# Performance work log

Hardware: AMD Instinct MI355X
Metric: run time of the kernel (lower is better)

## Reference

```python
import jax, jax.numpy as jnp
import numpy as np

N_HEAD = 16


def setup_inputs() -> dict:
    key = jax.random.key(0)
    ks = jax.random.split(key, 6)
    B, T, H = 4, 2048, 1024
    inp = jax.random.normal(ks[0], (B, T, H), dtype=jnp.float32)
    # padding mask: valid prefix of random length in [T//2, T] per batch row
    lengths = jax.random.randint(ks[1], (B, 1), T // 2, T + 1)
    mask = jnp.arange(T)[None, :] < lengths  # (B, T) bool
    s = 0.02
    w_qkv = jax.random.normal(ks[2], (H, 3 * H), dtype=jnp.float32) * s
    b_qkv = jax.random.normal(ks[3], (3 * H,), dtype=jnp.float32) * s
    w_out = jax.random.normal(ks[4], (H, H), dtype=jnp.float32) * s
    b_out = jax.random.normal(ks[5], (H,), dtype=jnp.float32) * s
    return {"input": inp, "mask": mask, "w_qkv": w_qkv, "b_qkv": b_qkv,
            "w_out": w_out, "b_out": b_out}


def reference(input, mask, w_qkv, b_qkv, w_out, b_out):
    B, T, H = input.shape
    hd = H // N_HEAD
    qkv = input @ w_qkv + b_qkv                       # (B, T, 3H)
    q, k, v = jnp.split(qkv, 3, axis=-1)
    # (B, T, H) -> (B, nh, T, hd)
    q = q.reshape(B, T, N_HEAD, hd).transpose(0, 2, 1, 3)
    k = k.reshape(B, T, N_HEAD, hd).transpose(0, 2, 1, 3)
    v = v.reshape(B, T, N_HEAD, hd).transpose(0, 2, 1, 3)
    scores = jnp.einsum('bhqd,bhkd->bhqk', q, k) / jnp.sqrt(jnp.float32(hd))
    causal = jnp.tril(jnp.ones((T, T), dtype=bool))   # (T, T)
    full_mask = causal[None, None, :, :] & mask[:, None, None, :]  # (B,1,T,T) bcast over heads
    scores = jnp.where(full_mask, scores, -jnp.inf)
    attn = jax.nn.softmax(scores, axis=-1)            # (B, nh, T, T)
    o = jnp.einsum('bhqk,bhkd->bhqd', attn, v)        # (B, nh, T, hd)
    o = o.transpose(0, 2, 1, 3).reshape(B, T, H)
    return o @ w_out + b_out
```

## Files before the change

### kernel.cpp

```cpp
#include <hip/hip_runtime.h>
#include <math.h>

#define B_  4
#define T_  2048
#define H_  1024
#define NH  16
#define HD  64
#define H3  3072

typedef short bf16x8 __attribute__((ext_vector_type(8)));
typedef float f32x4  __attribute__((ext_vector_type(4)));

#define SC2F 0.18033688011112042f

__device__ __forceinline__ unsigned short f2bf(float f) {
    union { float f; unsigned u; } v; v.f = f;
    unsigned u = v.u;
    unsigned r = (u + 0x7fffu + ((u >> 16) & 1u)) >> 16;
    return (unsigned short)r;
}

__device__ __forceinline__ void gload_lds16(const void* g, void* l) {
    __builtin_amdgcn_global_load_lds(
        (const __attribute__((address_space(1))) unsigned*)g,
        (__attribute__((address_space(3))) unsigned*)l, 16, 0, 0);
}

__global__ void lengths_kernel(const void* mask, int* lengths) {
    int b = blockIdx.x;
    int t = threadIdx.x;
    const unsigned* mu = (const unsigned*)mask;
    bool is_byte = (mu[0] == 0x01010101u);
    int cnt = 0;
    if (is_byte) {
        const unsigned char* m8 = (const unsigned char*)mask;
        for (int i = t; i < T_; i += 256) cnt += (m8[b * T_ + i] != 0);
    } else {
        const unsigned* m32 = (const unsigned*)mask;
        for (int i = t; i < T_; i += 256) cnt += (m32[b * T_ + i] != 0);
    }
    __shared__ int red[256];
    red[t] = cnt;
    __syncthreads();
    for (int s = 128; s > 0; s >>= 1) {
        if (t < s) red[t] += red[t + s];
        __syncthreads();
    }
    if (t == 0) lengths[b] = red[0];
}

__global__ void convert_bf16_kernel(const float* __restrict__ x,
                                    unsigned short* __restrict__ y, int n) {
    int i = (blockIdx.x * 256 + threadIdx.x) * 4;
    if (i < n) {
        float4 v = *(const float4*)(x + i);
        ushort4 o;
        o.x = f2bf(v.x); o.y = f2bf(v.y); o.z = f2bf(v.z); o.w = f2bf(v.w);
        *(ushort4*)(y + i) = o;
    }
}

__global__ void transpose_bf16_kernel(const float* __restrict__ in,
                                      unsigned short* __restrict__ out,
                                      int K, int N) {
    __shared__ unsigned short tile[32][33];
    int kb = blockIdx.y * 32, nb = blockIdx.x * 32;
    int tx = threadIdx.x, ty = threadIdx.y;
    for (int i = 0; i < 32; i += 8)
        tile[ty + i][tx] = f2bf(in[(long)(kb + ty + i) * N + nb + tx]);
    __syncthreads();
    for (int i = 0; i < 32; i += 8)
        out[(long)(nb + ty + i) * K + kb + tx] = tile[tx][ty + i];
}

__global__ void vtranspose_kernel(const unsigned short* __restrict__ QKV,
                                  unsigned short* __restrict__ Vt) {
    int idx = blockIdx.x;
    int tt = idx & 31, bh = idx >> 5;
    int b = bh >> 4, h = bh & 15;
    __shared__ unsigned short Ls[64][72];
    int tid = threadIdx.x;
    {
        int row = tid >> 2, cb = (tid & 3) * 16;
        const unsigned short* src = QKV + ((long)(b * T_ + tt * 64 + row)) * H3 + 2 * H_ + h * HD + cb;
        *(float4*)(&Ls[row][cb])     = *(const float4*)(src);
        *(float4*)(&Ls[row][cb + 8]) = *(const float4*)(src + 8);
    }
    __syncthreads();
    {
        int d = tid >> 2, cb = (tid & 3) * 16;
        __align__(16) unsigned short tmp[16];
#pragma unroll
        for (int e = 0; e < 16; e++) tmp[e] = Ls[cb + e][d];
        unsigned short* dst = Vt + ((long)(bh * 64 + d)) * T_ + tt * 64 + cb;
        *(float4*)(dst)     = *(const float4*)(tmp);
        *(float4*)(dst + 8) = *(const float4*)(tmp + 8);
    }
}

template <bool BF16_OUT, bool KSCALE>
__global__ __launch_bounds__(256) void gemm_kernel(
    const unsigned short* __restrict__ A,
    const unsigned short* __restrict__ Bt,
    const float* __restrict__ bias,
    void* __restrict__ C,
    int M, int N, int K)
{
    __shared__ unsigned short Asm[128][64];
    __shared__ unsigned short Bsm[128][64];

    int tn = blockIdx.x * 128, tm = blockIdx.y * 128;
    int tid = threadIdx.x;
    int wid = tid >> 6, lane = tid & 63, quad = lane >> 4, lr = lane & 15;
    int wm = (wid & 1) * 64, wn = (wid >> 1) * 64;

    int rl = lane >> 3, cs = (lane & 7) ^ rl;
    const unsigned short* aP = A  + (long)(tm + wid * 32 + rl) * K + cs * 8;
    const unsigned short* bP = Bt + (long)(tn + wid * 32 + rl) * K + cs * 8;
    int xk = lr & 7;

    f32x4 acc[4][4] = {};

    for (int k0 = 0; k0 < K; k0 += 64) {
        __syncthreads();
#pragma unroll
        for (int t = 0; t < 4; t++) {
            gload_lds16(aP + (long)t * 8 * K + k0, &Asm[wid * 32 + t * 8][0]);
            gload_lds16(bP + (long)t * 8 * K + k0, &Bsm[wid * 32 + t * 8][0]);
        }
        __syncthreads();

#pragma unroll
        for (int hh = 0; hh < 2; hh++) {
            int pc = ((hh * 4 + quad) ^ xk) * 8;
            bf16x8 af[4], bfv[4];
#pragma unroll
            for (int i = 0; i < 4; i++) af[i]  = *(const bf16x8*)(&Asm[wm + i * 16 + lr][pc]);
#pragma unroll
            for (int j = 0; j < 4; j++) bfv[j] = *(const bf16x8*)(&Bsm[wn + j * 16 + lr][pc]);
#pragma unroll
            for (int i = 0; i < 4; i++)
#pragma unroll
                for (int j = 0; j < 4; j++)
                    acc[i][j] = __builtin_amdgcn_mfma_f32_16x16x32_bf16(af[i], bfv[j], acc[i][j], 0, 0, 0);
        }
    }

#pragma unroll
    for (int i = 0; i < 4; i++)
#pragma unroll
        for (int j = 0; j < 4; j++) {
            int col = tn + wn + j * 16 + lr;
            float bs = bias[col];
            bool ks = KSCALE && (col >= H_) && (col < 2 * H_);
#pragma unroll
            for (int r = 0; r < 4; r++) {
                int row = tm + wm + i * 16 + quad * 4 + r;
                float v = acc[i][j][r] + bs;
                if (ks) v *= SC2F;
                if (BF16_OUT)
                    ((unsigned short*)C)[(long)row * N + col] = f2bf(v);
                else
                    ((float*)C)[(long)row * N + col] = v;
            }
        }
}

__global__ __launch_bounds__(256) void attn_kernel(
    const unsigned short* __restrict__ QKV,
    const unsigned short* __restrict__ Vt,
    const int* __restrict__ lengths,
    unsigned short* __restrict__ O)
{
    int idx = blockIdx.x;
    int bh = idx & 63;
    int pr = idx >> 6;
    int b = bh >> 4, h = bh & 15;
    int len = lengths[b];

    int tid = threadIdx.x;
    int wid = tid >> 6, lane = tid & 63, quad = lane >> 4, lr = lane & 15;

    __shared__ unsigned short Qs[128][72];
    __shared__ unsigned short Ks[64][72];
    __shared__ unsigned short Vts[64][72];

    const long qkv_base = (long)b * T_ * H3;
    int srow = tid >> 2, scb = (tid & 3) * 16;

    for (int pass = 0; pass < 2; pass++) {
        int qt = pass ? pr : (15 - pr);
        int q0 = qt * 128;

        __syncthreads();
        {
            int row = tid >> 1, cb = (tid & 1) * 32;
            const unsigned short* src = QKV + qkv_base + (long)(q0 + row) * H3 + h * HD + cb;
#pragma unroll
            for (int i = 0; i < 4; i++)
                *(float4*)(&Qs[row][cb + i * 8]) = *(const float4*)(src + i * 8);
        }
        __syncthreads();

        bf16x8 qf[2][2];
#pragma unroll
        for (int nq = 0; nq < 2; nq++)
#pragma unroll
            for (int ks = 0; ks < 2; ks++)
                qf[nq][ks] = *(const bf16x8*)(&Qs[wid * 32 + nq * 16 + lr][ks * 32 + quad * 8]);

        float l_i[2] = { 0.f, 0.f };
        f32x4 Oacc[4][2] = {};

        int kmax = min(q0 + 127, len - 1);
        int n_kt = (kmax >> 6) + 1;
        int q_wave_lo = q0 + wid * 32;
        int q_wave_hi = q_wave_lo + 31;
        int myq[2] = { q_wave_lo + lr, q_wave_lo + 16 + lr };

        const unsigned short* kp = QKV + qkv_base + (long)srow * H3 + H_ + h * HD + scb;
        const unsigned short* vp = Vt + ((long)(bh * 64 + srow)) * T_ + scb;

        for (int kt = 0; kt < n_kt; kt++) {
            __syncthreads();
            *(float4*)(&Ks[srow][scb])      = *(const float4*)(kp);
            *(float4*)(&Ks[srow][scb + 8])  = *(const float4*)(kp + 8);
            *(float4*)(&Vts[srow][scb])     = *(const float4*)(vp);
            *(float4*)(&Vts[srow][scb + 8]) = *(const float4*)(vp + 8);
            kp += (long)64 * H3;
            vp += 64;
            __syncthreads();

            int k_lo = kt * 64;
            if (k_lo > q_wave_hi || k_lo >= len) continue;

            f32x4 Sacc[4][2] = {};
#pragma unroll
            for (int ks = 0; ks < 2; ks++) {
#pragma unroll
                for (int mt = 0; mt < 4; mt++) {
                    bf16x8 kf = *(const bf16x8*)(&Ks[mt * 16 + lr][ks * 32 + quad * 8]);
                    Sacc[mt][0] = __builtin_amdgcn_mfma_f32_16x16x32_bf16(kf, qf[0][ks], Sacc[mt][0], 0, 0, 0);
                    Sacc[mt][1] = __builtin_amdgcn_mfma_f32_16x16x32_bf16(kf, qf[1][ks], Sacc[mt][1], 0, 0, 0);
                }
            }

            bool full = (k_lo + 63 <= q_wave_lo) && (k_lo + 63 < len);
            float rs[2] = { 0.f, 0.f };
            unsigned pk[4][2][2];
#pragma unroll
            for (int mt = 0; mt < 4; mt++)
#pragma unroll
                for (int nq = 0; nq < 2; nq++) {
                    float p[4];
#pragma unroll
                    for (int r = 0; r < 4; r++) {
                        float s = Sacc[mt][nq][r];
                        if (!full) {
                            int key = k_lo + mt * 16 + quad * 4 + r;
                            bool ok = (key <= myq[nq]) && (key < len);
                            s = ok ? s : -INFINITY;
                        }
                        p[r] = __builtin_amdgcn_exp2f(s);
                        rs[nq] += p[r];
                    }
                    pk[mt][nq][0] = __builtin_amdgcn_perm(__float_as_uint(p[1]), __float_as_uint(p[0]), 0x07060302);
                    pk[mt][nq][1] = __builtin_amdgcn_perm(__float_as_uint(p[3]), __float_as_uint(p[2]), 0x07060302);
                }

#pragma unroll
            for (int nq = 0; nq < 2; nq++) {
                float v = rs[nq];
                v += __shfl_xor(v, 16);
                v += __shfl_xor(v, 32);
                l_i[nq] += v;
            }

            int src0 = ((quad & 1) * 2) * 16 + lr;
            int src1 = src0 + 16;
            bool hi = (quad >> 1) != 0;
#pragma unroll
            for (int ks = 0; ks < 2; ks++) {
                bf16x8 vf[4];
#pragma unroll
                for (int md = 0; md < 4; md++)
                    vf[md] = *(const bf16x8*)(&Vts[md * 16 + lr][ks * 32 + quad * 8]);
#pragma unroll
                for (int nq = 0; nq < 2; nq++) {
                    unsigned w0a = (unsigned)__shfl((int)pk[ks * 2][nq][0], src0);
                    unsigned w0b = (unsigned)__shfl((int)pk[ks * 2 + 1][nq][0], src0);
                    unsigned w1a = (unsigned)__shfl((int)pk[ks * 2][nq][1], src0);
                    unsigned w1b = (unsigned)__shfl((int)pk[ks * 2 + 1][nq][1], src0);
                    unsigned w2a = (unsigned)__shfl((int)pk[ks * 2][nq][0], src1);
                    unsigned w2b = (unsigned)__shfl((int)pk[ks * 2 + 1][nq][0], src1);
                    unsigned w3a = (unsigned)__shfl((int)pk[ks * 2][nq][1], src1);
                    unsigned w3b = (unsigned)__shfl((int)pk[ks * 2 + 1][nq][1], src1);
                    union { unsigned w[4]; bf16x8 v; } bu;
                    bu.w[0] = hi ? w0b : w0a;
                    bu.w[1] = hi ? w1b : w1a;
                    bu.w[2] = hi ? w2b : w2a;
                    bu.w[3] = hi ? w3b : w3a;
#pragma unroll
                    for (int md = 0; md < 4; md++)
                        Oacc[md][nq] = __builtin_amdgcn_mfma_f32_16x16x32_bf16(vf[md], bu.v, Oacc[md][nq], 0, 0, 0);
                }
            }
        }

        {
            float inv[2] = { 1.f / l_i[0], 1.f / l_i[1] };
#pragma unroll
            for (int nq = 0; nq < 2; nq++)
#pragma unroll
                for (int md = 0; md < 4; md++)
#pragma unroll
                    for (int rp = 0; rp < 2; rp++) {
                        float e0 = Oacc[md][nq][rp * 2]     * inv[nq];
                        float e1 = Oacc[md][nq][rp * 2 + 1] * inv[nq];
                        unsigned w = __builtin_amdgcn_perm(__float_as_uint(e1), __float_as_uint(e0), 0x07060302);
                        *(unsigned*)(&Qs[wid * 32 + nq * 16 + lr][md * 16 + quad * 4 + rp * 2]) = w;
                    }
            __asm__ volatile("s_waitcnt lgkmcnt(0)" ::: "memory");
            int row = lane >> 1, cb = (lane & 1) * 32;
            long tok = (long)b * T_ + q0 + wid * 32 + row;
#pragma unroll
            for (int i = 0; i < 4; i++) {
                float4 v = *(const float4*)(&Qs[wid * 32 + row][cb + i * 8]);
                *(float4*)(&O[tok * H_ + h * HD + cb + i * 8]) = v;
            }
        }
    }
}

extern "C" void kernel_launch(void* const* d_in, const int* in_sizes, int n_in,
                              void* d_out, int out_size, void* d_ws, size_t ws_size,
                              hipStream_t stream) {
    const float* X    = (const float*)d_in[0];
    const void*  mask = d_in[1];
    const float* Wqkv = (const float*)d_in[2];
    const float* bqkv = (const float*)d_in[3];
    const float* Wout = (const float*)d_in[4];
    const float* bout = (const float*)d_in[5];

    char* ws = (char*)d_ws;
    int* lengths          = (int*)ws;
    unsigned short* WqkvT = (unsigned short*)(ws + 256);
    unsigned short* WoutT = WqkvT + (long)H3 * H_;
    unsigned short* QKV   = WoutT + (long)H_ * H_;
    unsigned short* Xbf   = QKV + (long)B_ * T_ * H3;
    unsigned short* Vt    = Xbf + (long)B_ * T_ * H_;
    unsigned short* Obf   = Xbf;

    const int M = B_ * T_;

    lengths_kernel<<<B_, 256, 0, stream>>>(mask, lengths);
    convert_bf16_kernel<<<(M * H_ / 4 + 255) / 256, 256, 0, stream>>>(X, Xbf, M * H_);
    transpose_bf16_kernel<<<dim3(H3 / 32, H_ / 32), dim3(32, 8), 0, stream>>>(Wqkv, WqkvT, H_, H3);
    transpose_bf16_kernel<<<dim3(H_ / 32, H_ / 32), dim3(32, 8), 0, stream>>>(Wout, WoutT, H_, H_);
    gemm_kernel<true, true><<<dim3(H3 / 128, M / 128), 256, 0, stream>>>(Xbf, WqkvT, bqkv, QKV, M, H3, H_);
    vtranspose_kernel<<<B_ * NH * (T_ / 64), 256, 0, stream>>>(QKV, Vt);
    attn_kernel<<<B_ * NH * 8, 256, 0, stream>>>(QKV, Vt, lengths, Obf);
    gemm_kernel<false, false><<<dim3(H_ / 128, M / 128), 256, 0, stream>>>(Obf, WoutT, bout, d_out, M, H_, H_);
}
```

Baseline: 297.7 us.

## Fuse V transpose into QKV GEMM epilogue and double-buffer attention K/V tiles

The QKV GEMM now writes the V columns directly into a transposed Vt layout in its epilogue, which removes the separate vtranspose kernel and its extra pass over memory. The GEMM k-step is cut from 64 to 32 and drops the XOR swizzle on shared memory, which may add LDS bank conflicts and more barriers per unit of work. The attention kernel double-buffers K/V tiles with register prefetch so there is one barrier per tile instead of two. It also replaces the shuffle-based P repacking with 16x16x16 MFMAs that consume the softmax output layout directly.

```diff
diff --git a/kernel.cpp b/kernel.cpp
--- a/kernel.cpp
+++ b/kernel.cpp
@@ -9,6 +9,7 @@
 #define H3  3072
 
 typedef short bf16x8 __attribute__((ext_vector_type(8)));
+typedef short bf16x4 __attribute__((ext_vector_type(4)));
 typedef float f32x4  __attribute__((ext_vector_type(4)));
 
 #define SC2F 0.18033688011112042f
@@ -24,6 +25,19 @@
     __builtin_amdgcn_global_load_lds(
         (const __attribute__((address_space(1))) unsigned*)g,
         (__attribute__((address_space(3))) unsigned*)l, 16, 0, 0);
+}
+
+__device__ __forceinline__ f32x4 mfma_16x16x16_bf16(bf16x4 a, bf16x4 b, f32x4 c) {
+#if __has_builtin(__builtin_amdgcn_mfma_f32_16x16x16_bf16)
+    return __builtin_amdgcn_mfma_f32_16x16x16_bf16(a, b, c, 0, 0, 0);
+#elif __has_builtin(__builtin_amdgcn_mfma_f32_16x16x16bf16_1k)
+    return __builtin_amdgcn_mfma_f32_16x16x16bf16_1k(a, b, c, 0, 0, 0);
+#else
+    f32x4 d;
+    asm volatile("v_mfma_f32_16x16x16_bf16 %0, %1, %2, %3"
+                 : "=v"(d) : "v"(a), "v"(b), "v"(c));
+    return d;
+#endif
 }
 
 __global__ void lengths_kernel(const void* mask, int* lengths) {
@@ -73,77 +87,66 @@
         out[(long)(nb + ty + i) * K + kb + tx] = tile[tx][ty + i];
 }
 
-__global__ void vtranspose_kernel(const unsigned short* __restrict__ QKV,
-                                  unsigned short* __restrict__ Vt) {
-    int idx = blockIdx.x;
-    int tt = idx & 31, bh = idx >> 5;
-    int b = bh >> 4, h = bh & 15;
-    __shared__ unsigned short Ls[64][72];
-    int tid = threadIdx.x;
-    {
-        int row = tid >> 2, cb = (tid & 3) * 16;
-        const unsigned short* src = QKV + ((long)(b * T_ + tt * 64 + row)) * H3 + 2 * H_ + h * HD + cb;
-        *(float4*)(&Ls[row][cb])     = *(const float4*)(src);
-        *(float4*)(&Ls[row][cb + 8]) = *(const float4*)(src + 8);
-    }
-    __syncthreads();
-    {
-        int d = tid >> 2, cb = (tid & 3) * 16;
-        __align__(16) unsigned short tmp[16];
-#pragma unroll
-        for (int e = 0; e < 16; e++) tmp[e] = Ls[cb + e][d];
-        unsigned short* dst = Vt + ((long)(bh * 64 + d)) * T_ + tt * 64 + cb;
-        *(float4*)(dst)     = *(const float4*)(tmp);
-        *(float4*)(dst + 8) = *(const float4*)(tmp + 8);
-    }
-}
-
-template <bool BF16_OUT, bool KSCALE>
+template <bool BF16_OUT, bool KSCALE, bool VSPLIT>
 __global__ __launch_bounds__(256) void gemm_kernel(
     const unsigned short* __restrict__ A,
     const unsigned short* __restrict__ Bt,
     const float* __restrict__ bias,
     void* __restrict__ C,
+    unsigned short* __restrict__ Vt,
     int M, int N, int K)
 {
-    __shared__ unsigned short Asm[128][64];
-    __shared__ unsigned short Bsm[128][64];
+    __shared__ unsigned short Asm[128][32];
+    __shared__ unsigned short Bsm[128][32];
 
     int tn = blockIdx.x * 128, tm = blockIdx.y * 128;
     int tid = threadIdx.x;
     int wid = tid >> 6, lane = tid & 63, quad = lane >> 4, lr = lane & 15;
     int wm = (wid & 1) * 64, wn = (wid >> 1) * 64;
-
-    int rl = lane >> 3, cs = (lane & 7) ^ rl;
-    const unsigned short* aP = A  + (long)(tm + wid * 32 + rl) * K + cs * 8;
-    const unsigned short* bP = Bt + (long)(tn + wid * 32 + rl) * K + cs * 8;
-    int xk = lr & 7;
+    int grow = lane >> 2, gcol = (lane & 3) * 8;
 
     f32x4 acc[4][4] = {};
 
-    for (int k0 = 0; k0 < K; k0 += 64) {
-        __syncthreads();
-#pragma unroll
-        for (int t = 0; t < 4; t++) {
-            gload_lds16(aP + (long)t * 8 * K + k0, &Asm[wid * 32 + t * 8][0]);
-            gload_lds16(bP + (long)t * 8 * K + k0, &Bsm[wid * 32 + t * 8][0]);
-        }
-        __syncthreads();
-
-#pragma unroll
-        for (int hh = 0; hh < 2; hh++) {
-            int pc = ((hh * 4 + quad) ^ xk) * 8;
-            bf16x8 af[4], bfv[4];
-#pragma unroll
-            for (int i = 0; i < 4; i++) af[i]  = *(const bf16x8*)(&Asm[wm + i * 16 + lr][pc]);
-#pragma unroll
-            for (int j = 0; j < 4; j++) bfv[j] = *(const bf16x8*)(&Bsm[wn + j * 16 + lr][pc]);
-#pragma unroll
-            for (int i = 0; i < 4; i++)
-#pragma unroll
-                for (int j = 0; j < 4; j++)
-                    acc[i][j] = __builtin_amdgcn_mfma_f32_16x16x32_bf16(af[i], bfv[j], acc[i][j], 0, 0, 0);
-        }
+    for (int k0 = 0; k0 < K; k0 += 32) {
+        __syncthreads();
+#pragma unroll
+        for (int t = 0; t < 2; t++) {
+            int ar = wid * 32 + t * 16 + grow;
+            gload_lds16(A  + (long)(tm + ar) * K + k0 + gcol, &Asm[wid * 32 + t * 16][0]);
+            gload_lds16(Bt + (long)(tn + ar) * K + k0 + gcol, &Bsm[wid * 32 + t * 16][0]);
+        }
+        __syncthreads();
+
+        bf16x8 af[4], bfv[4];
+#pragma unroll
+        for (int i = 0; i < 4; i++) af[i]  = *(const bf16x8*)(&Asm[wm + i * 16 + lr][quad * 8]);
+#pragma unroll
+        for (int j = 0; j < 4; j++) bfv[j] = *(const bf16x8*)(&Bsm[wn + j * 16 + lr][quad * 8]);
+#pragma unroll
+        for (int i = 0; i < 4; i++)
+#pragma unroll
+            for (int j = 0; j < 4; j++)
+                acc[i][j] = __builtin_amdgcn_mfma_f32_16x16x32_bf16(af[i], bfv[j], acc[i][j], 0, 0, 0);
+    }
+
+    if (VSPLIT && tn >= 2 * H_) {
+#pragma unroll
+        for (int i = 0; i < 4; i++)
+#pragma unroll
+            for (int j = 0; j < 4; j++) {
+                int col = tn + wn + j * 16 + lr;
+                float bs = bias[col];
+                int feat = col - 2 * H_;
+                int tok0 = tm + wm + i * 16 + quad * 4;
+                int bb = tok0 >> 11;
+                unsigned d0 = (unsigned)f2bf(acc[i][j][0] + bs) |
+                              ((unsigned)f2bf(acc[i][j][1] + bs) << 16);
+                unsigned d1 = (unsigned)f2bf(acc[i][j][2] + bs) |
+                              ((unsigned)f2bf(acc[i][j][3] + bs) << 16);
+                unsigned short* dst = Vt + ((long)(bb * 1024 + feat)) * T_ + (tok0 & (T_ - 1));
+                *(uint2*)dst = make_uint2(d0, d1);
+            }
+        return;
     }
 
 #pragma unroll
@@ -182,11 +185,13 @@
     int wid = tid >> 6, lane = tid & 63, quad = lane >> 4, lr = lane & 15;
 
     __shared__ unsigned short Qs[128][72];
-    __shared__ unsigned short Ks[64][72];
-    __shared__ unsigned short Vts[64][72];
+    __shared__ unsigned short Kd[2][64][72];
+    __shared__ unsigned short Vd[2][64][72];
 
     const long qkv_base = (long)b * T_ * H3;
     int srow = tid >> 2, scb = (tid & 3) * 16;
+    const unsigned short* kbase = QKV + qkv_base + (long)srow * H3 + H_ + h * HD + scb;
+    const unsigned short* vbase = Vt + ((long)(bh * 64 + srow)) * T_ + scb;
 
     for (int pass = 0; pass < 2; pass++) {
         int qt = pass ? pr : (15 - pr);
@@ -199,6 +204,16 @@
 #pragma unroll
             for (int i = 0; i < 4; i++)
                 *(float4*)(&Qs[row][cb + i * 8]) = *(const float4*)(src + i * 8);
+        }
+        {
+            float4 k0 = *(const float4*)(kbase);
+            float4 k1 = *(const float4*)(kbase + 8);
+            float4 v0 = *(const float4*)(vbase);
+            float4 v1 = *(const float4*)(vbase + 8);
+            *(float4*)(&Kd[0][srow][scb])     = k0;
+            *(float4*)(&Kd[0][srow][scb + 8]) = k1;
+            *(float4*)(&Vd[0][srow][scb])     = v0;
+            *(float4*)(&Vd[0][srow][scb + 8]) = v1;
         }
         __syncthreads();
 
@@ -218,93 +233,87 @@
         int q_wave_hi = q_wave_lo + 31;
         int myq[2] = { q_wave_lo + lr, q_wave_lo + 16 + lr };
 
-        const unsigned short* kp = QKV + qkv_base + (long)srow * H3 + H_ + h * HD + scb;
-        const unsigned short* vp = Vt + ((long)(bh * 64 + srow)) * T_ + scb;
+        const unsigned short* kp = kbase + (long)64 * H3;
+        const unsigned short* vp = vbase + 64;
 
         for (int kt = 0; kt < n_kt; kt++) {
+            int cur = kt & 1;
+            float4 pk0, pk1, pv0, pv1;
+            bool pf = (kt + 1 < n_kt);
+            if (pf) {
+                pk0 = *(const float4*)(kp);
+                pk1 = *(const float4*)(kp + 8);
+                pv0 = *(const float4*)(vp);
+                pv1 = *(const float4*)(vp + 8);
+                kp += (long)64 * H3;
+                vp += 64;
+            }
+
+            int k_lo = kt * 64;
+            if (!(k_lo > q_wave_hi || k_lo >= len)) {
+                f32x4 Sacc[4][2] = {};
+#pragma unroll
+                for (int ks = 0; ks < 2; ks++) {
+#pragma unroll
+                    for (int mt = 0; mt < 4; mt++) {
+                        bf16x8 kf = *(const bf16x8*)(&Kd[cur][mt * 16 + lr][ks * 32 + quad * 8]);
+                        Sacc[mt][0] = __builtin_amdgcn_mfma_f32_16x16x32_bf16(kf, qf[0][ks], Sacc[mt][0], 0, 0, 0);
+                        Sacc[mt][1] = __builtin_amdgcn_mfma_f32_16x16x32_bf16(kf, qf[1][ks], Sacc[mt][1], 0, 0, 0);
+                    }
+                }
+
+                bool full = (k_lo + 63 <= q_wave_lo) && (k_lo + 63 < len);
+                float rs[2] = { 0.f, 0.f };
+                unsigned pkk[4][2][2];
+#pragma unroll
+                for (int mt = 0; mt < 4; mt++)
+#pragma unroll
+                    for (int nq = 0; nq < 2; nq++) {
+                        float p[4];
+#pragma unroll
+                        for (int r = 0; r < 4; r++) {
+                            float s = Sacc[mt][nq][r];
+                            if (!full) {
+                                int key = k_lo + mt * 16 + quad * 4 + r;
+                                bool ok = (key <= myq[nq]) && (key < len);
+                                s = ok ? s : -INFINITY;
+                            }
+                            p[r] = __builtin_amdgcn_exp2f(s);
+                            rs[nq] += p[r];
+                        }
+                        pkk[mt][nq][0] = __builtin_amdgcn_perm(__float_as_uint(p[1]), __float_as_uint(p[0]), 0x07060302);
+                        pkk[mt][nq][1] = __builtin_amdgcn_perm(__float_as_uint(p[3]), __float_as_uint(p[2]), 0x07060302);
+                    }
+
+#pragma unroll
+                for (int nq = 0; nq < 2; nq++) {
+                    float v = rs[nq];
+                    v += __shfl_xor(v, 16);
+                    v += __shfl_xor(v, 32);
+                    l_i[nq] += v;
+                }
+
+#pragma unroll
+                for (int mt = 0; mt < 4; mt++) {
+                    union { unsigned u[2]; bf16x4 v; } bu[2];
+                    bu[0].u[0] = pkk[mt][0][0]; bu[0].u[1] = pkk[mt][0][1];
+                    bu[1].u[0] = pkk[mt][1][0]; bu[1].u[1] = pkk[mt][1][1];
+#pragma unroll
+                    for (int md = 0; md < 4; md++) {
+                        bf16x4 vf = *(const bf16x4*)(&Vd[cur][md * 16 + lr][mt * 16 + quad * 4]);
+                        Oacc[md][0] = mfma_16x16x16_bf16(vf, bu[0].v, Oacc[md][0]);
+                        Oacc[md][1] = mfma_16x16x16_bf16(vf, bu[1].v, Oacc[md][1]);
+                    }
+                }
+            }
+
+            if (pf) {
+                *(float4*)(&Kd[cur ^ 1][srow][scb])     = pk0;
+                *(float4*)(&Kd[cur ^ 1][srow][scb + 8]) = pk1;
+                *(float4*)(&Vd[cur ^ 1][srow][scb])     = pv0;
+                *(float4*)(&Vd[cur ^ 1][srow][scb + 8]) = pv1;
+            }
             __syncthreads();
-            *(float4*)(&Ks[srow][scb])      = *(const float4*)(kp);
-            *(float4*)(&Ks[srow][scb + 8])  = *(const float4*)(kp + 8);
-            *(float4*)(&Vts[srow][scb])     = *(const float4*)(vp);
-            *(float4*)(&Vts[srow][scb + 8]) = *(const float4*)(vp + 8);
-            kp += (long)64 * H3;
-            vp += 64;
-            __syncthreads();
-
-            int k_lo = kt * 64;
-            if (k_lo > q_wave_hi || k_lo >= len) continue;
-
-            f32x4 Sacc[4][2] = {};
-#pragma unroll
-            for (int ks = 0; ks < 2; ks++) {
-#pragma unroll
-                for (int mt = 0; mt < 4; mt++) {
-                    bf16x8 kf = *(const bf16x8*)(&Ks[mt * 16 + lr][ks * 32 + quad * 8]);
-                    Sacc[mt][0] = __builtin_amdgcn_mfma_f32_16x16x32_bf16(kf, qf[0][ks], Sacc[mt][0], 0, 0, 0);
-                    Sacc[mt][1] = __builtin_amdgcn_mfma_f32_16x16x32_bf16(kf, qf[1][ks], Sacc[mt][1], 0, 0, 0);
-                }
-            }
-
-            bool full = (k_lo + 63 <= q_wave_lo) && (k_lo + 63 < len);
-            float rs[2] = { 0.f, 0.f };
-            unsigned pk[4][2][2];
-#pragma unroll
-            for (int mt = 0; mt < 4; mt++)
-#pragma unroll
-                for (int nq = 0; nq < 2; nq++) {
-                    float p[4];
-#pragma unroll
-                    for (int r = 0; r < 4; r++) {
-                        float s = Sacc[mt][nq][r];
-                        if (!full) {
-                            int key = k_lo + mt * 16 + quad * 4 + r;
-                            bool ok = (key <= myq[nq]) && (key < len);
-                            s = ok ? s : -INFINITY;
-                        }
-                        p[r] = __builtin_amdgcn_exp2f(s);
-                        rs[nq] += p[r];
-                    }
-                    pk[mt][nq][0] = __builtin_amdgcn_perm(__float_as_uint(p[1]), __float_as_uint(p[0]), 0x07060302);
-                    pk[mt][nq][1] = __builtin_amdgcn_perm(__float_as_uint(p[3]), __float_as_uint(p[2]), 0x07060302);
-                }
-
-#pragma unroll
-            for (int nq = 0; nq < 2; nq++) {
-                float v = rs[nq];
-                v += __shfl_xor(v, 16);
-                v += __shfl_xor(v, 32);
-                l_i[nq] += v;
-            }
-
-            int src0 = ((quad & 1) * 2) * 16 + lr;
-            int src1 = src0 + 16;
-            bool hi = (quad >> 1) != 0;
-#pragma unroll
-            for (int ks = 0; ks < 2; ks++) {
-                bf16x8 vf[4];
-#pragma unroll
-                for (int md = 0; md < 4; md++)
-                    vf[md] = *(const bf16x8*)(&Vts[md * 16 + lr][ks * 32 + quad * 8]);
-#pragma unroll
-                for (int nq = 0; nq < 2; nq++) {
-                    unsigned w0a = (unsigned)__shfl((int)pk[ks * 2][nq][0], src0);
-                    unsigned w0b = (unsigned)__shfl((int)pk[ks * 2 + 1][nq][0], src0);
-                    unsigned w1a = (unsigned)__shfl((int)pk[ks * 2][nq][1], src0);
-                    unsigned w1b = (unsigned)__shfl((int)pk[ks * 2 + 1][nq][1], src0);
-                    unsigned w2a = (unsigned)__shfl((int)pk[ks * 2][nq][0], src1);
-                    unsigned w2b = (unsigned)__shfl((int)pk[ks * 2 + 1][nq][0], src1);
-                    unsigned w3a = (unsigned)__shfl((int)pk[ks * 2][nq][1], src1);
-                    unsigned w3b = (unsigned)__shfl((int)pk[ks * 2 + 1][nq][1], src1);
-                    union { unsigned w[4]; bf16x8 v; } bu;
-                    bu.w[0] = hi ? w0b : w0a;
-                    bu.w[1] = hi ? w1b : w1a;
-                    bu.w[2] = hi ? w2b : w2a;
-                    bu.w[3] = hi ? w3b : w3a;
-#pragma unroll
-                    for (int md = 0; md < 4; md++)
-                        Oacc[md][nq] = __builtin_amdgcn_mfma_f32_16x16x32_bf16(vf[md], bu.v, Oacc[md][nq], 0, 0, 0);
-                }
-            }
         }
 
         {
@@ -357,8 +366,9 @@
     convert_bf16_kernel<<<(M * H_ / 4 + 255) / 256, 256, 0, stream>>>(X, Xbf, M * H_);
     transpose_bf16_kernel<<<dim3(H3 / 32, H_ / 32), dim3(32, 8), 0, stream>>>(Wqkv, WqkvT, H_, H3);
     transpose_bf16_kernel<<<dim3(H_ / 32, H_ / 32), dim3(32, 8), 0, stream>>>(Wout, WoutT, H_, H_);
-    gemm_kernel<true, true><<<dim3(H3 / 128, M / 128), 256, 0, stream>>>(Xbf, WqkvT, bqkv, QKV, M, H3, H_);
-    vtranspose_kernel<<<B_ * NH * (T_ / 64), 256, 0, stream>>>(QKV, Vt);
+    gemm_kernel<true, true, true><<<dim3(H3 / 128, M / 128), 256, 0, stream>>>(
+        Xbf, WqkvT, bqkv, QKV, Vt, M, H3, H_);
     attn_kernel<<<B_ * NH * 8, 256, 0, stream>>>(QKV, Vt, lengths, Obf);
-    gemm_kernel<false, false><<<dim3(H_ / 128, M / 128), 256, 0, stream>>>(Obf, WoutT, bout, d_out, M, H_, H_);
-}
+    gemm_kernel<false, false, false><<<dim3(H_ / 128, M / 128), 256, 0, stream>>>(
+        Obf, WoutT, bout, d_out, nullptr, M, H_, H_);
+}
```

Result: no change. 300.0 us (+0.8%).
